# Kernel tuning notes

Hardware: AMD Instinct MI355X
Metric: run time of the kernel (lower is better)

Reference implementation:

```python
import jax, jax.numpy as jnp
import numpy as np

UFEAT_DIM = 512
EFEAT_DIM = 256
BATCH = 64
PNUM_UNIT = 1024
PNUM_ENEMY = 1024


def setup_inputs() -> dict:
    key = jax.random.key(0)
    k1, k2, k3, k4, k5 = jax.random.split(key, 5)
    ufeat = jax.random.normal(k1, (BATCH, PNUM_UNIT, UFEAT_DIM), dtype=jnp.float32)
    efeat = jax.random.normal(k2, (BATCH, PNUM_ENEMY, EFEAT_DIM), dtype=jnp.float32)
    num_enemy = jax.random.randint(k3, (BATCH,), 0, PNUM_ENEMY, dtype=jnp.int64)
    # weight_norm(Linear, dim=None): W = g * v / ||v||_F, g scalar
    v = jax.random.normal(k4, (EFEAT_DIM, UFEAT_DIM), dtype=jnp.float32) * (1.0 / np.sqrt(UFEAT_DIM))
    g = jnp.asarray(jnp.linalg.norm(v), dtype=jnp.float32)  # init g = ||v||
    b = jax.random.normal(k5, (EFEAT_DIM,), dtype=jnp.float32) * 0.01
    return {"ufeat": ufeat, "efeat": efeat, "num_enemy": num_enemy, "v": v, "g": g, "b": b}


def reference(ufeat, efeat, num_enemy, v, g, b):
    # weight-normed linear (dim=None -> Frobenius norm) + ReLU projection
    W = g * v / jnp.linalg.norm(v)                       # [efeat_dim, ufeat_dim]
    proj = jax.nn.relu(ufeat @ W.T + b)                  # [B, U, efeat_dim]
    # batched dot-product scores (fused matmul instead of repeat+mul+sum)
    norm = jnp.float32(np.sqrt(EFEAT_DIM))
    logit = jnp.einsum('bue,bne->bun', proj, efeat) / norm  # [B, U, N]
    # real-enemy mask: mask[b, n] = 1 iff n < num_enemy[b]
    mask = (jnp.arange(PNUM_ENEMY)[None, :] < num_enemy[:, None]).astype(logit.dtype)
    logit = logit - (1.0 - mask)[:, None, :] * 1e9       # masking bias (uniform if all masked)
    prob = jax.nn.softmax(logit, axis=2)
    return prob
```

## Files before the change

kernel.cpp:

```cpp
#include <hip/hip_runtime.h>
#include <hip/hip_bf16.h>

#define UF 512
#define EF 256
#define NB 64
#define NU 1024
#define NEN 1024

typedef __attribute__((ext_vector_type(8))) short short8;
typedef __attribute__((ext_vector_type(4))) float floatx4;

typedef unsigned short ushort_t;

__device__ inline short2 cvt2(float a, float b) {
    __hip_bfloat162 h = __float22bfloat162_rn(make_float2(a, b));
    union { __hip_bfloat162 h; short2 s; } u;
    u.h = h;
    return u.s;
}

__device__ inline short8 cvt8(float4 x, float4 y) {
    union { short8 v; short2 s[4]; } u;
    u.s[0] = cvt2(x.x, x.y);
    u.s[1] = cvt2(x.z, x.w);
    u.s[2] = cvt2(y.x, y.y);
    u.s[3] = cvt2(y.z, y.w);
    return u.v;
}

__device__ inline ushort_t f2bfbits(float f) {
    unsigned u = __float_as_uint(f);
    u += 0x7FFFu + ((u >> 16) & 1u);
    return (ushort_t)(u >> 16);
}

__global__ void knorm(const float* __restrict__ v, float* __restrict__ ws0) {
    int t = blockIdx.x * 256 + threadIdx.x;
    float2 x = ((const float2*)v)[t];
    float s = x.x * x.x + x.y * x.y;
    #pragma unroll
    for (int m = 1; m < 64; m <<= 1) s += __shfl_xor(s, m);
    __shared__ float ls[4];
    int w = threadIdx.x >> 6;
    if ((threadIdx.x & 63) == 0) ls[w] = s;
    __syncthreads();
    if (threadIdx.x == 0) atomicAdd(ws0, ls[0] + ls[1] + ls[2] + ls[3]);
}

__global__ void kconv(const float* __restrict__ v, const float* __restrict__ g,
                      const float* __restrict__ ef, const float* __restrict__ ws0,
                      ushort_t* __restrict__ wsW, ushort_t* __restrict__ wsE) {
    int bid = blockIdx.x;
    if (bid < 128) {
        int t = bid * 256 + threadIdx.x;
        float s = g[0] * rsqrtf(ws0[0]);
        float4 x = ((const float4*)v)[t];
        short2 a = cvt2(x.x * s, x.y * s);
        short2 b = cvt2(x.z * s, x.w * s);
        ushort4 o;
        o.x = (ushort_t)a.x; o.y = (ushort_t)a.y; o.z = (ushort_t)b.x; o.w = (ushort_t)b.y;
        ((ushort4*)wsW)[t] = o;
    } else {
        long t = (long)(bid - 128) * 256 + threadIdx.x;
        float4 x = ((const float4*)ef)[t];
        short2 a = cvt2(x.x, x.y);
        short2 b = cvt2(x.z, x.w);
        ushort4 o;
        o.x = (ushort_t)a.x; o.y = (ushort_t)a.y; o.z = (ushort_t)b.x; o.w = (ushort_t)b.y;
        ((ushort4*)wsE)[t] = o;
    }
}

__launch_bounds__(256, 2)
__global__ void kgemm1(const float* __restrict__ A, const ushort_t* __restrict__ W,
                       const float* __restrict__ bias, ushort_t* __restrict__ P) {
    const int tid = threadIdx.x;
    const int w = tid >> 6, L = tid & 63;
    const int rA = L & 15, q = L >> 4;
    const long mt = (long)blockIdx.x * 32;

    floatx4 acc[2][4];
    #pragma unroll
    for (int t = 0; t < 2; t++)
        #pragma unroll
        for (int n = 0; n < 4; n++) acc[t][n] = (floatx4){0.f, 0.f, 0.f, 0.f};

    const float* a0 = A + (mt + rA) * UF + q * 8;
    const float* a1 = A + (mt + 16 + rA) * UF + q * 8;
    const ushort_t* wp0 = W + (long)(w * 64 + 0 * 16 + rA) * UF + q * 8;
    const ushort_t* wp1 = W + (long)(w * 64 + 1 * 16 + rA) * UF + q * 8;
    const ushort_t* wp2 = W + (long)(w * 64 + 2 * 16 + rA) * UF + q * 8;
    const ushort_t* wp3 = W + (long)(w * 64 + 3 * 16 + rA) * UF + q * 8;

    #pragma unroll 2
    for (int s = 0; s < 16; s++) {
        const int ko = s * 32;
        float4 x0 = *(const float4*)(a0 + ko);
        float4 y0 = *(const float4*)(a0 + ko + 4);
        float4 x1 = *(const float4*)(a1 + ko);
        float4 y1 = *(const float4*)(a1 + ko + 4);
        short8 af0 = cvt8(x0, y0);
        short8 af1 = cvt8(x1, y1);
        short8 b0 = *(const short8*)(wp0 + ko);
        short8 b1 = *(const short8*)(wp1 + ko);
        short8 b2 = *(const short8*)(wp2 + ko);
        short8 b3 = *(const short8*)(wp3 + ko);
        acc[0][0] = __builtin_amdgcn_mfma_f32_16x16x32_bf16(af0, b0, acc[0][0], 0, 0, 0);
        acc[1][0] = __builtin_amdgcn_mfma_f32_16x16x32_bf16(af1, b0, acc[1][0], 0, 0, 0);
        acc[0][1] = __builtin_amdgcn_mfma_f32_16x16x32_bf16(af0, b1, acc[0][1], 0, 0, 0);
        acc[1][1] = __builtin_amdgcn_mfma_f32_16x16x32_bf16(af1, b1, acc[1][1], 0, 0, 0);
        acc[0][2] = __builtin_amdgcn_mfma_f32_16x16x32_bf16(af0, b2, acc[0][2], 0, 0, 0);
        acc[1][2] = __builtin_amdgcn_mfma_f32_16x16x32_bf16(af1, b2, acc[1][2], 0, 0, 0);
        acc[0][3] = __builtin_amdgcn_mfma_f32_16x16x32_bf16(af0, b3, acc[0][3], 0, 0, 0);
        acc[1][3] = __builtin_amdgcn_mfma_f32_16x16x32_bf16(af1, b3, acc[1][3], 0, 0, 0);
    }

    #pragma unroll
    for (int n = 0; n < 4; n++) {
        const int col = w * 64 + n * 16 + rA;
        const float bv = bias[col];
        #pragma unroll
        for (int t = 0; t < 2; t++) {
            #pragma unroll
            for (int i = 0; i < 4; i++) {
                float val = acc[t][n][i] + bv;
                val = fmaxf(val, 0.f);
                const long row = mt + t * 16 + q * 4 + i;
                P[row * EF + col] = f2bfbits(val);
            }
        }
    }
}

__launch_bounds__(256, 2)
__global__ void kattn(const ushort_t* __restrict__ P, const ushort_t* __restrict__ E,
                      const int* __restrict__ nen, float* __restrict__ out) {
    const int tid = threadIdx.x;
    const int w = tid >> 6, L = tid & 63;
    const int rA = L & 15, q = L >> 4;
    const int bid = blockIdx.x;
    const int b = ((bid & 7) << 3) | ((bid >> 3) & 7);
    const int ut = bid >> 6;
    const int ne = nen[b];

    const ushort_t* prow = P + (long)(b * NU + ut * 32 + rA) * EF + q * 8;
    short8 af[2][8];
    #pragma unroll
    for (int t = 0; t < 2; t++)
        #pragma unroll
        for (int s = 0; s < 8; s++)
            af[t][s] = *(const short8*)(prow + t * 16 * EF + s * 32);

    floatx4 acc[2][16];
    float psum[2][4];
    #pragma unroll
    for (int t = 0; t < 2; t++)
        #pragma unroll
        for (int i = 0; i < 4; i++) psum[t][i] = 0.f;

    const ushort_t* erow = E + (long)(b * NEN + w * 256 + rA) * EF + q * 8;

    #pragma unroll
    for (int ns = 0; ns < 16; ns++) {
        const ushort_t* ep = erow + (long)ns * 16 * EF;
        floatx4 c0 = (floatx4){0.f, 0.f, 0.f, 0.f};
        floatx4 c1 = (floatx4){0.f, 0.f, 0.f, 0.f};
        #pragma unroll
        for (int h = 0; h < 2; h++) {
            short8 bf[4];
            #pragma unroll
            for (int s = 0; s < 4; s++) bf[s] = *(const short8*)(ep + (h * 4 + s) * 32);
            #pragma unroll
            for (int s = 0; s < 4; s++) {
                c0 = __builtin_amdgcn_mfma_f32_16x16x32_bf16(af[0][h * 4 + s], bf[s], c0, 0, 0, 0);
                c1 = __builtin_amdgcn_mfma_f32_16x16x32_bf16(af[1][h * 4 + s], bf[s], c1, 0, 0, 0);
            }
        }
        const int col = w * 256 + ns * 16 + rA;
        const bool on = col < ne;
        #pragma unroll
        for (int i = 0; i < 4; i++) {
            float e0 = on ? __expf(c0[i] * 0.0625f) : 0.f;
            float e1 = on ? __expf(c1[i] * 0.0625f) : 0.f;
            c0[i] = e0; c1[i] = e1;
            psum[0][i] += e0; psum[1][i] += e1;
        }
        acc[0][ns] = c0;
        acc[1][ns] = c1;
    }

    #pragma unroll
    for (int t = 0; t < 2; t++)
        #pragma unroll
        for (int i = 0; i < 4; i++) {
            float s = psum[t][i];
            s += __shfl_xor(s, 1);
            s += __shfl_xor(s, 2);
            s += __shfl_xor(s, 4);
            s += __shfl_xor(s, 8);
            psum[t][i] = s;
        }
    __shared__ float lsum[4][32];
    if (rA == 0) {
        #pragma unroll
        for (int t = 0; t < 2; t++)
            #pragma unroll
            for (int i = 0; i < 4; i++)
                lsum[w][t * 16 + q * 4 + i] = psum[t][i];
    }
    __syncthreads();

    float inv[2][4];
    #pragma unroll
    for (int t = 0; t < 2; t++)
        #pragma unroll
        for (int i = 0; i < 4; i++) {
            const int r = t * 16 + q * 4 + i;
            const float tot = lsum[0][r] + lsum[1][r] + lsum[2][r] + lsum[3][r];
            inv[t][i] = (ne > 0) ? (1.f / tot) : 0.f;
        }

    const float uni = 1.f / 1024.f;
    float* orow = out + ((long)(b * NU + ut * 32)) * (long)NEN + w * 256;
    #pragma unroll
    for (int ns = 0; ns < 16; ns++) {
        #pragma unroll
        for (int t = 0; t < 2; t++) {
            #pragma unroll
            for (int i = 0; i < 4; i++) {
                const int u = t * 16 + q * 4 + i;
                const float val = (ne == 0) ? uni : acc[t][ns][i] * inv[t][i];
                orow[(long)u * NEN + ns * 16 + rA] = val;
            }
        }
    }
}

extern "C" void kernel_launch(void* const* d_in, const int* in_sizes, int n_in,
                              void* d_out, int out_size, void* d_ws, size_t ws_size,
                              hipStream_t stream) {
    (void)in_sizes; (void)n_in; (void)out_size; (void)ws_size;
    const float* ufeat = (const float*)d_in[0];
    const float* efeat = (const float*)d_in[1];
    const int*   nen   = (const int*)d_in[2];
    const float* v     = (const float*)d_in[3];
    const float* g     = (const float*)d_in[4];
    const float* bias  = (const float*)d_in[5];
    float* out = (float*)d_out;

    float*    ws0 = (float*)d_ws;
    ushort_t* wsW = (ushort_t*)((char*)d_ws + 1024);
    ushort_t* wsE = (ushort_t*)((char*)d_ws + (1u << 20));
    ushort_t* wsP = (ushort_t*)((char*)d_ws + (1u << 20) + (32u << 20));

    hipMemsetAsync(d_ws, 0, 256, stream);
    knorm<<<256, 256, 0, stream>>>(v, ws0);
    kconv<<<16512, 256, 0, stream>>>(v, g, efeat, ws0, wsW, wsE);
    kgemm1<<<2048, 256, 0, stream>>>(ufeat, wsW, bias, wsP);
    kattn<<<2048, 256, 0, stream>>>(wsP, wsE, nen, out);
}
```

Before: 611.8 us.

## Skip masked enemy columns in conversion and attention, halve attention tile rows

The efeat conversion now loads and converts only rows with n < num_enemy, and the attention kernel skips MFMA work and E loads for 16-column groups that lie entirely beyond num_enemy. The attention tile shrinks from 32 to 16 unit rows, which doubles the grid to 4096 blocks. Occupancy is raised to 3 blocks per SM, and blocks are remapped so each XCD handles 8 whole batches for better L2 locality of E. Masking is valid per the semantics, but unconverted E rows are left uninitialised in the workspace and must never be read, and the smaller tile reloads each E tile twice as often.

Result: slower. 652.3 us (+6.6%).

```diff
diff --git a/kernel.cpp b/kernel.cpp
--- a/kernel.cpp
+++ b/kernel.cpp
@@ -49,6 +49,7 @@
 
 __global__ void kconv(const float* __restrict__ v, const float* __restrict__ g,
                       const float* __restrict__ ef, const float* __restrict__ ws0,
+                      const int* __restrict__ nen,
                       ushort_t* __restrict__ wsW, ushort_t* __restrict__ wsE) {
     int bid = blockIdx.x;
     if (bid < 128) {
@@ -62,12 +63,17 @@
         ((ushort4*)wsW)[t] = o;
     } else {
         long t = (long)(bid - 128) * 256 + threadIdx.x;
-        float4 x = ((const float4*)ef)[t];
-        short2 a = cvt2(x.x, x.y);
-        short2 b = cvt2(x.z, x.w);
-        ushort4 o;
-        o.x = (ushort_t)a.x; o.y = (ushort_t)a.y; o.z = (ushort_t)b.x; o.w = (ushort_t)b.y;
-        ((ushort4*)wsE)[t] = o;
+        int row = (int)(t >> 6);
+        int n = row & (NEN - 1);
+        int b = row >> 10;
+        if (n < nen[b]) {
+            float4 x = ((const float4*)ef)[t];
+            short2 a = cvt2(x.x, x.y);
+            short2 c = cvt2(x.z, x.w);
+            ushort4 o;
+            o.x = (ushort_t)a.x; o.y = (ushort_t)a.y; o.z = (ushort_t)c.x; o.w = (ushort_t)c.y;
+            ((ushort4*)wsE)[t] = o;
+        }
     }
 }
 
@@ -132,106 +138,91 @@
     }
 }
 
-__launch_bounds__(256, 2)
+__launch_bounds__(256, 3)
 __global__ void kattn(const ushort_t* __restrict__ P, const ushort_t* __restrict__ E,
                       const int* __restrict__ nen, float* __restrict__ out) {
     const int tid = threadIdx.x;
     const int w = tid >> 6, L = tid & 63;
     const int rA = L & 15, q = L >> 4;
     const int bid = blockIdx.x;
-    const int b = ((bid & 7) << 3) | ((bid >> 3) & 7);
-    const int ut = bid >> 6;
+    const int xcd = bid & 7;
+    const int idx = bid >> 3;
+    const int b = xcd * 8 + (idx >> 6);
+    const int ut = idx & 63;
     const int ne = nen[b];
 
-    const ushort_t* prow = P + (long)(b * NU + ut * 32 + rA) * EF + q * 8;
-    short8 af[2][8];
-    #pragma unroll
-    for (int t = 0; t < 2; t++)
-        #pragma unroll
-        for (int s = 0; s < 8; s++)
-            af[t][s] = *(const short8*)(prow + t * 16 * EF + s * 32);
-
-    floatx4 acc[2][16];
-    float psum[2][4];
-    #pragma unroll
-    for (int t = 0; t < 2; t++)
-        #pragma unroll
-        for (int i = 0; i < 4; i++) psum[t][i] = 0.f;
+    const ushort_t* prow = P + (long)(b * NU + ut * 16 + rA) * EF + q * 8;
+    short8 af[8];
+    #pragma unroll
+    for (int s = 0; s < 8; s++) af[s] = *(const short8*)(prow + s * 32);
+
+    floatx4 acc[16];
+    #pragma unroll
+    for (int ns = 0; ns < 16; ns++) acc[ns] = (floatx4){0.f, 0.f, 0.f, 0.f};
+    float psum[4] = {0.f, 0.f, 0.f, 0.f};
 
     const ushort_t* erow = E + (long)(b * NEN + w * 256 + rA) * EF + q * 8;
 
     #pragma unroll
     for (int ns = 0; ns < 16; ns++) {
-        const ushort_t* ep = erow + (long)ns * 16 * EF;
-        floatx4 c0 = (floatx4){0.f, 0.f, 0.f, 0.f};
-        floatx4 c1 = (floatx4){0.f, 0.f, 0.f, 0.f};
-        #pragma unroll
-        for (int h = 0; h < 2; h++) {
-            short8 bf[4];
+        const int col0 = w * 256 + ns * 16;
+        if (col0 < ne) {
+            const ushort_t* ep = erow + (long)ns * 16 * EF;
+            floatx4 c = (floatx4){0.f, 0.f, 0.f, 0.f};
             #pragma unroll
-            for (int s = 0; s < 4; s++) bf[s] = *(const short8*)(ep + (h * 4 + s) * 32);
-            #pragma unroll
-            for (int s = 0; s < 4; s++) {
-                c0 = __builtin_amdgcn_mfma_f32_16x16x32_bf16(af[0][h * 4 + s], bf[s], c0, 0, 0, 0);
-                c1 = __builtin_amdgcn_mfma_f32_16x16x32_bf16(af[1][h * 4 + s], bf[s], c1, 0, 0, 0);
+            for (int h = 0; h < 2; h++) {
+                short8 bf[4];
+                #pragma unroll
+                for (int s = 0; s < 4; s++) bf[s] = *(const short8*)(ep + (h * 4 + s) * 32);
+                #pragma unroll
+                for (int s = 0; s < 4; s++)
+                    c = __builtin_amdgcn_mfma_f32_16x16x32_bf16(af[h * 4 + s], bf[s], c, 0, 0, 0);
             }
-        }
-        const int col = w * 256 + ns * 16 + rA;
-        const bool on = col < ne;
-        #pragma unroll
-        for (int i = 0; i < 4; i++) {
-            float e0 = on ? __expf(c0[i] * 0.0625f) : 0.f;
-            float e1 = on ? __expf(c1[i] * 0.0625f) : 0.f;
-            c0[i] = e0; c1[i] = e1;
-            psum[0][i] += e0; psum[1][i] += e1;
-        }
-        acc[0][ns] = c0;
-        acc[1][ns] = c1;
-    }
-
-    #pragma unroll
-    for (int t = 0; t < 2; t++)
-        #pragma unroll
-        for (int i = 0; i < 4; i++) {
-            float s = psum[t][i];
-            s += __shfl_xor(s, 1);
-            s += __shfl_xor(s, 2);
-            s += __shfl_xor(s, 4);
-            s += __shfl_xor(s, 8);
-            psum[t][i] = s;
-        }
-    __shared__ float lsum[4][32];
-    if (rA == 0) {
-        #pragma unroll
-        for (int t = 0; t < 2; t++)
-            #pragma unroll
-            for (int i = 0; i < 4; i++)
-                lsum[w][t * 16 + q * 4 + i] = psum[t][i];
-    }
-    __syncthreads();
-
-    float inv[2][4];
-    #pragma unroll
-    for (int t = 0; t < 2; t++)
-        #pragma unroll
-        for (int i = 0; i < 4; i++) {
-            const int r = t * 16 + q * 4 + i;
-            const float tot = lsum[0][r] + lsum[1][r] + lsum[2][r] + lsum[3][r];
-            inv[t][i] = (ne > 0) ? (1.f / tot) : 0.f;
-        }
-
-    const float uni = 1.f / 1024.f;
-    float* orow = out + ((long)(b * NU + ut * 32)) * (long)NEN + w * 256;
-    #pragma unroll
-    for (int ns = 0; ns < 16; ns++) {
-        #pragma unroll
-        for (int t = 0; t < 2; t++) {
+            const int col = col0 + rA;
+            const bool on = col < ne;
             #pragma unroll
             for (int i = 0; i < 4; i++) {
-                const int u = t * 16 + q * 4 + i;
-                const float val = (ne == 0) ? uni : acc[t][ns][i] * inv[t][i];
-                orow[(long)u * NEN + ns * 16 + rA] = val;
+                float e = on ? __expf(c[i] * 0.0625f) : 0.f;
+                c[i] = e;
+                psum[i] += e;
             }
+            acc[ns] = c;
+        }
+    }
+
+    #pragma unroll
+    for (int i = 0; i < 4; i++) {
+        float s = psum[i];
+        s += __shfl_xor(s, 1);
+        s += __shfl_xor(s, 2);
+        s += __shfl_xor(s, 4);
+        s += __shfl_xor(s, 8);
+        psum[i] = s;
+    }
+    __shared__ float lsum[4][16];
+    if (rA == 0) {
+        #pragma unroll
+        for (int i = 0; i < 4; i++) lsum[w][q * 4 + i] = psum[i];
+    }
+    __syncthreads();
+
+    float inv[4];
+    #pragma unroll
+    for (int i = 0; i < 4; i++) {
+        const int r = q * 4 + i;
+        const float tot = lsum[0][r] + lsum[1][r] + lsum[2][r] + lsum[3][r];
+        inv[i] = (ne > 0) ? (1.f / tot) : 0.f;
+    }
+
+    const float uni = 1.f / 1024.f;
+    float* orow = out + ((long)(b * NU + ut * 16)) * (long)NEN + w * 256;
+    #pragma unroll
+    for (int ns = 0; ns < 16; ns++) {
+        #pragma unroll
+        for (int i = 0; i < 4; i++) {
+            const int u = q * 4 + i;
+            const float val = (ne == 0) ? uni : acc[ns][i] * inv[i];
+            orow[(long)u * NEN + ns * 16 + rA] = val;
         }
     }
 }
@@ -255,7 +246,7 @@
 
     hipMemsetAsync(d_ws, 0, 256, stream);
     knorm<<<256, 256, 0, stream>>>(v, ws0);
-    kconv<<<16512, 256, 0, stream>>>(v, g, efeat, ws0, wsW, wsE);
+    kconv<<<16512, 256, 0, stream>>>(v, g, efeat, ws0, nen, wsW, wsE);
     kgemm1<<<2048, 256, 0, stream>>>(ufeat, wsW, bias, wsP);
-    kattn<<<2048, 256, 0, stream>>>(wsP, wsE, nen, out);
-}
+    kattn<<<4096, 256, 0, stream>>>(wsP, wsE, nen, out);
+}
```

## Skip masked enemy columns, enlarge GEMM1 tile, use nontemporal loads and stores

Applied to the files above, without the earlier changes.

The efeat conversion kernel and the attention kernel now skip enemy rows at or beyond num_enemy. Conversion only writes valid rows, and attention interleaves columns across waves so each 16-column MFMA group past the limit is skipped while work stays balanced between waves. GEMM1 now computes 64 rows per block instead of 32, which reuses the W fragments over more rows, and it reads ufeat with nontemporal loads. Output stores are nontemporal and the block-to-batch mapping changes, which drops the earlier interleaved swizzle and may change L2 locality.

New measurement: 594.1 us. -2.9%, faster.

```diff
diff --git a/kernel.cpp b/kernel.cpp
--- a/kernel.cpp
+++ b/kernel.cpp
@@ -19,12 +19,12 @@
     return u.s;
 }
 
-__device__ inline short8 cvt8(float4 x, float4 y) {
+__device__ inline short8 cvt8v(floatx4 x, floatx4 y) {
     union { short8 v; short2 s[4]; } u;
-    u.s[0] = cvt2(x.x, x.y);
-    u.s[1] = cvt2(x.z, x.w);
-    u.s[2] = cvt2(y.x, y.y);
-    u.s[3] = cvt2(y.z, y.w);
+    u.s[0] = cvt2(x[0], x[1]);
+    u.s[1] = cvt2(x[2], x[3]);
+    u.s[2] = cvt2(y[0], y[1]);
+    u.s[3] = cvt2(y[2], y[3]);
     return u.v;
 }
 
@@ -49,6 +49,7 @@
 
 __global__ void kconv(const float* __restrict__ v, const float* __restrict__ g,
                       const float* __restrict__ ef, const float* __restrict__ ws0,
+                      const int* __restrict__ nen,
                       ushort_t* __restrict__ wsW, ushort_t* __restrict__ wsE) {
     int bid = blockIdx.x;
     if (bid < 128) {
@@ -62,12 +63,17 @@
         ((ushort4*)wsW)[t] = o;
     } else {
         long t = (long)(bid - 128) * 256 + threadIdx.x;
-        float4 x = ((const float4*)ef)[t];
-        short2 a = cvt2(x.x, x.y);
-        short2 b = cvt2(x.z, x.w);
-        ushort4 o;
-        o.x = (ushort_t)a.x; o.y = (ushort_t)a.y; o.z = (ushort_t)b.x; o.w = (ushort_t)b.y;
-        ((ushort4*)wsE)[t] = o;
+        int row = (int)(t >> 6);
+        int n = row & (NEN - 1);
+        int b = row >> 10;
+        if (n < nen[b]) {
+            float4 x = ((const float4*)ef)[t];
+            short2 a = cvt2(x.x, x.y);
+            short2 c = cvt2(x.z, x.w);
+            ushort4 o;
+            o.x = (ushort_t)a.x; o.y = (ushort_t)a.y; o.z = (ushort_t)c.x; o.w = (ushort_t)c.y;
+            ((ushort4*)wsE)[t] = o;
+        }
     }
 }
 
@@ -77,42 +83,39 @@
     const int tid = threadIdx.x;
     const int w = tid >> 6, L = tid & 63;
     const int rA = L & 15, q = L >> 4;
-    const long mt = (long)blockIdx.x * 32;
-
-    floatx4 acc[2][4];
-    #pragma unroll
-    for (int t = 0; t < 2; t++)
-        #pragma unroll
-        for (int n = 0; n < 4; n++) acc[t][n] = (floatx4){0.f, 0.f, 0.f, 0.f};
-
-    const float* a0 = A + (mt + rA) * UF + q * 8;
-    const float* a1 = A + (mt + 16 + rA) * UF + q * 8;
-    const ushort_t* wp0 = W + (long)(w * 64 + 0 * 16 + rA) * UF + q * 8;
-    const ushort_t* wp1 = W + (long)(w * 64 + 1 * 16 + rA) * UF + q * 8;
-    const ushort_t* wp2 = W + (long)(w * 64 + 2 * 16 + rA) * UF + q * 8;
-    const ushort_t* wp3 = W + (long)(w * 64 + 3 * 16 + rA) * UF + q * 8;
+    const long mt = (long)blockIdx.x * 64;
+
+    floatx4 acc[4][4];
+    #pragma unroll
+    for (int m = 0; m < 4; m++)
+        #pragma unroll
+        for (int n = 0; n < 4; n++) acc[m][n] = (floatx4){0.f, 0.f, 0.f, 0.f};
+
+    const float* ap[4];
+    const ushort_t* wp[4];
+    #pragma unroll
+    for (int m = 0; m < 4; m++) ap[m] = A + (mt + m * 16 + rA) * UF + q * 8;
+    #pragma unroll
+    for (int n = 0; n < 4; n++) wp[n] = W + (long)(w * 64 + n * 16 + rA) * UF + q * 8;
 
     #pragma unroll 2
     for (int s = 0; s < 16; s++) {
         const int ko = s * 32;
-        float4 x0 = *(const float4*)(a0 + ko);
-        float4 y0 = *(const float4*)(a0 + ko + 4);
-        float4 x1 = *(const float4*)(a1 + ko);
-        float4 y1 = *(const float4*)(a1 + ko + 4);
-        short8 af0 = cvt8(x0, y0);
-        short8 af1 = cvt8(x1, y1);
-        short8 b0 = *(const short8*)(wp0 + ko);
-        short8 b1 = *(const short8*)(wp1 + ko);
-        short8 b2 = *(const short8*)(wp2 + ko);
-        short8 b3 = *(const short8*)(wp3 + ko);
-        acc[0][0] = __builtin_amdgcn_mfma_f32_16x16x32_bf16(af0, b0, acc[0][0], 0, 0, 0);
-        acc[1][0] = __builtin_amdgcn_mfma_f32_16x16x32_bf16(af1, b0, acc[1][0], 0, 0, 0);
-        acc[0][1] = __builtin_amdgcn_mfma_f32_16x16x32_bf16(af0, b1, acc[0][1], 0, 0, 0);
-        acc[1][1] = __builtin_amdgcn_mfma_f32_16x16x32_bf16(af1, b1, acc[1][1], 0, 0, 0);
-        acc[0][2] = __builtin_amdgcn_mfma_f32_16x16x32_bf16(af0, b2, acc[0][2], 0, 0, 0);
-        acc[1][2] = __builtin_amdgcn_mfma_f32_16x16x32_bf16(af1, b2, acc[1][2], 0, 0, 0);
-        acc[0][3] = __builtin_amdgcn_mfma_f32_16x16x32_bf16(af0, b3, acc[0][3], 0, 0, 0);
-        acc[1][3] = __builtin_amdgcn_mfma_f32_16x16x32_bf16(af1, b3, acc[1][3], 0, 0, 0);
+        short8 af[4];
+        #pragma unroll
+        for (int m = 0; m < 4; m++) {
+            floatx4 x = __builtin_nontemporal_load((const floatx4*)(ap[m] + ko));
+            floatx4 y = __builtin_nontemporal_load((const floatx4*)(ap[m] + ko + 4));
+            af[m] = cvt8v(x, y);
+        }
+        short8 bfr[4];
+        #pragma unroll
+        for (int n = 0; n < 4; n++) bfr[n] = *(const short8*)(wp[n] + ko);
+        #pragma unroll
+        for (int n = 0; n < 4; n++)
+            #pragma unroll
+            for (int m = 0; m < 4; m++)
+                acc[m][n] = __builtin_amdgcn_mfma_f32_16x16x32_bf16(af[m], bfr[n], acc[m][n], 0, 0, 0);
     }
 
     #pragma unroll
@@ -120,12 +123,12 @@
         const int col = w * 64 + n * 16 + rA;
         const float bv = bias[col];
         #pragma unroll
-        for (int t = 0; t < 2; t++) {
+        for (int m = 0; m < 4; m++) {
             #pragma unroll
             for (int i = 0; i < 4; i++) {
-                float val = acc[t][n][i] + bv;
+                float val = acc[m][n][i] + bv;
                 val = fmaxf(val, 0.f);
-                const long row = mt + t * 16 + q * 4 + i;
+                const long row = mt + m * 16 + q * 4 + i;
                 P[row * EF + col] = f2bfbits(val);
             }
         }
@@ -139,8 +142,8 @@
     const int w = tid >> 6, L = tid & 63;
     const int rA = L & 15, q = L >> 4;
     const int bid = blockIdx.x;
-    const int b = ((bid & 7) << 3) | ((bid >> 3) & 7);
-    const int ut = bid >> 6;
+    const int b = bid >> 5;
+    const int ut = bid & 31;
     const int ne = nen[b];
 
     const ushort_t* prow = P + (long)(b * NU + ut * 32 + rA) * EF + q * 8;
@@ -152,41 +155,48 @@
             af[t][s] = *(const short8*)(prow + t * 16 * EF + s * 32);
 
     floatx4 acc[2][16];
+    #pragma unroll
+    for (int t = 0; t < 2; t++)
+        #pragma unroll
+        for (int ns = 0; ns < 16; ns++) acc[t][ns] = (floatx4){0.f, 0.f, 0.f, 0.f};
     float psum[2][4];
     #pragma unroll
     for (int t = 0; t < 2; t++)
         #pragma unroll
         for (int i = 0; i < 4; i++) psum[t][i] = 0.f;
 
-    const ushort_t* erow = E + (long)(b * NEN + w * 256 + rA) * EF + q * 8;
+    const ushort_t* erow = E + (long)(b * NEN + w * 16 + rA) * EF + q * 8;
 
     #pragma unroll
     for (int ns = 0; ns < 16; ns++) {
-        const ushort_t* ep = erow + (long)ns * 16 * EF;
-        floatx4 c0 = (floatx4){0.f, 0.f, 0.f, 0.f};
-        floatx4 c1 = (floatx4){0.f, 0.f, 0.f, 0.f};
-        #pragma unroll
-        for (int h = 0; h < 2; h++) {
-            short8 bf[4];
-            #pragma unroll
-            for (int s = 0; s < 4; s++) bf[s] = *(const short8*)(ep + (h * 4 + s) * 32);
-            #pragma unroll
-            for (int s = 0; s < 4; s++) {
-                c0 = __builtin_amdgcn_mfma_f32_16x16x32_bf16(af[0][h * 4 + s], bf[s], c0, 0, 0, 0);
-                c1 = __builtin_amdgcn_mfma_f32_16x16x32_bf16(af[1][h * 4 + s], bf[s], c1, 0, 0, 0);
-            }
-        }
-        const int col = w * 256 + ns * 16 + rA;
-        const bool on = col < ne;
-        #pragma unroll
-        for (int i = 0; i < 4; i++) {
-            float e0 = on ? __expf(c0[i] * 0.0625f) : 0.f;
-            float e1 = on ? __expf(c1[i] * 0.0625f) : 0.f;
-            c0[i] = e0; c1[i] = e1;
-            psum[0][i] += e0; psum[1][i] += e1;
-        }
-        acc[0][ns] = c0;
-        acc[1][ns] = c1;
+        const int col0 = ns * 64 + w * 16;
+        if (col0 < ne) {
+            const ushort_t* ep = erow + (long)ns * 64 * EF;
+            floatx4 c0 = (floatx4){0.f, 0.f, 0.f, 0.f};
+            floatx4 c1 = (floatx4){0.f, 0.f, 0.f, 0.f};
+            #pragma unroll
+            for (int h = 0; h < 2; h++) {
+                short8 bf[4];
+                #pragma unroll
+                for (int s = 0; s < 4; s++) bf[s] = *(const short8*)(ep + (h * 4 + s) * 32);
+                #pragma unroll
+                for (int s = 0; s < 4; s++) {
+                    c0 = __builtin_amdgcn_mfma_f32_16x16x32_bf16(af[0][h * 4 + s], bf[s], c0, 0, 0, 0);
+                    c1 = __builtin_amdgcn_mfma_f32_16x16x32_bf16(af[1][h * 4 + s], bf[s], c1, 0, 0, 0);
+                }
+            }
+            const int col = col0 + rA;
+            const bool on = col < ne;
+            #pragma unroll
+            for (int i = 0; i < 4; i++) {
+                float e0 = on ? __expf(c0[i] * 0.0625f) : 0.f;
+                float e1 = on ? __expf(c1[i] * 0.0625f) : 0.f;
+                c0[i] = e0; c1[i] = e1;
+                psum[0][i] += e0; psum[1][i] += e1;
+            }
+            acc[0][ns] = c0;
+            acc[1][ns] = c1;
+        }
     }
 
     #pragma unroll
@@ -221,7 +231,7 @@
         }
 
     const float uni = 1.f / 1024.f;
-    float* orow = out + ((long)(b * NU + ut * 32)) * (long)NEN + w * 256;
+    float* orow = out + ((long)(b * NU + ut * 32)) * (long)NEN + w * 16;
     #pragma unroll
     for (int ns = 0; ns < 16; ns++) {
         #pragma unroll
@@ -230,7 +240,7 @@
             for (int i = 0; i < 4; i++) {
                 const int u = t * 16 + q * 4 + i;
                 const float val = (ne == 0) ? uni : acc[t][ns][i] * inv[t][i];
-                orow[(long)u * NEN + ns * 16 + rA] = val;
+                __builtin_nontemporal_store(val, &orow[(long)u * NEN + ns * 64 + rA]);
             }
         }
     }
@@ -255,7 +265,7 @@
 
     hipMemsetAsync(d_ws, 0, 256, stream);
     knorm<<<256, 256, 0, stream>>>(v, ws0);
-    kconv<<<16512, 256, 0, stream>>>(v, g, efeat, ws0, wsW, wsE);
-    kgemm1<<<2048, 256, 0, stream>>>(ufeat, wsW, bias, wsP);
+    kconv<<<16512, 256, 0, stream>>>(v, g, efeat, ws0, nen, wsW, wsE);
+    kgemm1<<<1024, 256, 0, stream>>>(ufeat, wsW, bias, wsP);
     kattn<<<2048, 256, 0, stream>>>(wsP, wsE, nen, out);
 }
```
